# Kernel optimization log

Hardware: AMD Instinct MI355X
Metric: run time of the kernel (lower is better)

Reference implementation:

```python
import jax, jax.numpy as jnp
import numpy as np


def setup_inputs() -> dict:
    key = jax.random.key(0)
    k1, k2, k3 = jax.random.split(key, 3)
    B, N, K, F, H = 4, 50000, 10, 128, 16
    x = jax.random.normal(k1, (B, N, K, F), dtype=jnp.float32)
    # xavier-like scales for learned params
    W = jax.random.normal(k2, (F, 4 * H), dtype=jnp.float32) * (1.0 / np.sqrt(F))
    a = jax.random.normal(k3, (4, H), dtype=jnp.float32) * 0.5
    return {"x": x, "W": W, "a": a}


def reference(x, W, a):
    # x: [B, N, K, F]; W: [F, 4H] (head-major blocks of 4); a: [4, H]
    B, N, K, F = x.shape
    H = a.shape[1]
    Wr = W.reshape(F, H, 4)                              # per-head projection
    hw = jnp.einsum('bnkf,fhd->bnkhd', x, Wr)            # [B,N,K,H,4]
    logits = jnp.einsum('bnkhd,dh->bnkh', hw, a)         # [B,N,K,H]
    attn = jax.nn.softmax(logits, axis=2)                # softmax over K neighbors
    out = jnp.einsum('bnkh,bnkhd->bnhd', attn, hw)       # [B,N,H,4]
    out = jax.nn.leaky_relu(out, negative_slope=0.2)
    out = out.reshape(B, N, H * 4)                       # concat over heads
    return out.transpose(0, 2, 1)                        # [B, 4H, N]
```

## Files before the change

kernel.cpp:

```cpp
#include <hip/hip_runtime.h>

typedef short bf16x8 __attribute__((ext_vector_type(8)));
typedef float f32x4 __attribute__((ext_vector_type(4)));

constexpr int Bc = 4;
constexpr int Nc = 50000;
constexpr int Kc = 10;
constexpr int Fc = 128;
constexpr int Hc = 16;
constexpr int Cc = 64;
constexpr int NODES = Bc * Nc;
constexpr int NPB = 8;
constexpr int ROWS = NPB * Kc;
constexpr int MT = ROWS / 16;
constexpr int BLK = 256;

constexpr int LDS_BYTES = 36864;
constexpr int WT_OFF = 20480;
constexpr int OL_OFF = 21760;

__device__ __forceinline__ unsigned short f2bf(float f) {
    unsigned u = __builtin_bit_cast(unsigned, f);
    return (unsigned short)((u + 0x7fffu + ((u >> 16) & 1u)) >> 16);
}

__global__ __launch_bounds__(256)
void prep_w(const float* __restrict__ W, unsigned short* __restrict__ wt) {
    const int t = threadIdx.x;
#pragma unroll
    for (int i = 0; i < 32; ++i) {
        const int flat = t + i * 256;
        const int c = flat & 63;
        const int f = flat >> 6;
        wt[c * 128 + (f ^ ((c & 7) << 3))] = f2bf(W[flat]);
    }
}

__global__ __launch_bounds__(BLK)
void gat_kernel(const float* __restrict__ x,
                const unsigned short* __restrict__ wt_ws,
                const float* __restrict__ a,
                float* __restrict__ out)
{
    __shared__ __align__(16) char smem[LDS_BYTES];

    const int t = threadIdx.x;

    {
        const float4* xg = reinterpret_cast<const float4*>(x + (size_t)blockIdx.x * (ROWS * Fc));
#pragma unroll
        for (int i = 0; i < (ROWS * Fc / 4) / BLK; ++i) {
            const int idx = t + i * BLK;
            const int row = idx >> 5;
            const int f4  = idx & 31;
            const float4 v = xg[idx];
            const unsigned lo = (unsigned)f2bf(v.x) | ((unsigned)f2bf(v.y) << 16);
            const unsigned hi = (unsigned)f2bf(v.z) | ((unsigned)f2bf(v.w) << 16);
            const int byt = (f4 * 8) ^ ((row & 7) << 4);
            *reinterpret_cast<uint2*>(smem + row * 256 + byt) = make_uint2(lo, hi);
        }
        const float4* wg = reinterpret_cast<const float4*>(wt_ws);
#pragma unroll
        for (int i = 0; i < 4; ++i)
            *reinterpret_cast<float4*>(smem + WT_OFF + t * 16 + i * 4096) = wg[t + i * BLK];
    }
    __syncthreads();

    const int w  = t >> 6;
    const int l  = t & 63;
    const int lr = l & 15;
    const int lk = l >> 4;

    bf16x8 bfrag[4];
    {
        const int c = w * 16 + lr;
        const char* wrow = smem + WT_OFF + c * 256;
        const int sw = (c & 7) << 4;
#pragma unroll
        for (int kc = 0; kc < 4; ++kc)
            bfrag[kc] = *reinterpret_cast<const bf16x8*>(wrow + ((kc * 64 + lk * 16) ^ sw));
    }

    f32x4 acc[MT];
#pragma unroll
    for (int m = 0; m < MT; ++m) acc[m] = (f32x4){0.f, 0.f, 0.f, 0.f};

#pragma unroll
    for (int m = 0; m < MT; ++m) {
        const int row = m * 16 + lr;
        const char* xrow = smem + row * 256;
        const int sw = (row & 7) << 4;
#pragma unroll
        for (int kc = 0; kc < 4; ++kc) {
            const bf16x8 af = *reinterpret_cast<const bf16x8*>(xrow + ((kc * 64 + lk * 16) ^ sw));
            acc[m] = __builtin_amdgcn_mfma_f32_16x16x32_bf16(af, bfrag[kc], acc[m], 0, 0, 0);
        }
    }
    __syncthreads();

    {
        float* hw = reinterpret_cast<float*>(smem);
        const int col = w * 16 + lr;
#pragma unroll
        for (int m = 0; m < MT; ++m) {
            const int rbase = m * 16 + lk * 4;
#pragma unroll
            for (int r = 0; r < 4; ++r)
                hw[(rbase + r) * 68 + col] = acc[m][r];
        }
    }
    __syncthreads();

    const float* hw = reinterpret_cast<const float*>(smem);
    float* ol = reinterpret_cast<float*>(smem + OL_OFF);
    if (t < NPB * Hc) {
        const int h  = t & 15;
        const int ln = t >> 4;
        const float ar0 = a[0 * Hc + h];
        const float ar1 = a[1 * Hc + h];
        const float ar2 = a[2 * Hc + h];
        const float ar3 = a[3 * Hc + h];

        float4 hv[Kc];
        float  lg[Kc];
        float  mx = -1e30f;
#pragma unroll
        for (int k = 0; k < Kc; ++k) {
            hv[k] = *reinterpret_cast<const float4*>(hw + (ln * Kc + k) * 68 + h * 4);
            lg[k] = fmaf(hv[k].x, ar0, fmaf(hv[k].y, ar1, fmaf(hv[k].z, ar2, hv[k].w * ar3)));
            mx = fmaxf(mx, lg[k]);
        }
        float lsum = 0.f, o0 = 0.f, o1 = 0.f, o2 = 0.f, o3 = 0.f;
#pragma unroll
        for (int k = 0; k < Kc; ++k) {
            const float p = __expf(lg[k] - mx);
            lsum += p;
            o0 = fmaf(p, hv[k].x, o0);
            o1 = fmaf(p, hv[k].y, o1);
            o2 = fmaf(p, hv[k].z, o2);
            o3 = fmaf(p, hv[k].w, o3);
        }
        const float inv = 1.f / lsum;
        o0 *= inv; o1 *= inv; o2 *= inv; o3 *= inv;
        o0 = fmaxf(o0, 0.2f * o0);
        o1 = fmaxf(o1, 0.2f * o1);
        o2 = fmaxf(o2, 0.2f * o2);
        o3 = fmaxf(o3, 0.2f * o3);
        *reinterpret_cast<float4*>(ol + ln * 68 + h * 4) = make_float4(o0, o1, o2, o3);
    }
    __syncthreads();

    if (t < 128) {
        const int c  = t >> 1;
        const int nq = t & 1;
        const int nb = blockIdx.x * NPB;
        const int b  = nb / Nc;
        const int n0 = nb - b * Nc;
        float4 v;
        v.x = ol[(nq * 4 + 0) * 68 + c];
        v.y = ol[(nq * 4 + 1) * 68 + c];
        v.z = ol[(nq * 4 + 2) * 68 + c];
        v.w = ol[(nq * 4 + 3) * 68 + c];
        *reinterpret_cast<float4*>(out + ((size_t)b * Cc + c) * Nc + n0 + nq * 4) = v;
    }
}

extern "C" void kernel_launch(void* const* d_in, const int* in_sizes, int n_in,
                              void* d_out, int out_size, void* d_ws, size_t ws_size,
                              hipStream_t stream) {
    const float* x = (const float*)d_in[0];
    const float* W = (const float*)d_in[1];
    const float* a = (const float*)d_in[2];
    float* out = (float*)d_out;
    unsigned short* wt = (unsigned short*)d_ws;

    prep_w<<<1, 256, 0, stream>>>(W, wt);
    gat_kernel<<<NODES / NPB, BLK, 0, stream>>>(x, wt, a, out);
}
```

Measured before the change: 233.6 us.

## Load x directly from global into MFMA fragments, skipping LDS staging

Each wave now reads its x rows straight from global memory into registers, converts them to bf16 and feeds the MFMA. The shared-memory staging pass and one barrier are gone. W is pre-laid out in fragment order so each lane loads its B fragments directly from global, and prep_w is spread across 32 blocks. Launch bounds request 4 blocks per CU. The trade-off is that every wave reads all 16 rows across lanes with 32-byte strided accesses, so global coalescing is weaker, and all four waves redundantly read the same x rows and lean on cache.

Measured after the change: 472.0 us. 2.02x slower.

```diff
diff --git a/kernel.cpp b/kernel.cpp
--- a/kernel.cpp
+++ b/kernel.cpp
@@ -15,57 +15,42 @@
 constexpr int MT = ROWS / 16;
 constexpr int BLK = 256;
 
-constexpr int LDS_BYTES = 36864;
-constexpr int WT_OFF = 20480;
-constexpr int OL_OFF = 21760;
-
 __device__ __forceinline__ unsigned short f2bf(float f) {
     unsigned u = __builtin_bit_cast(unsigned, f);
     return (unsigned short)((u + 0x7fffu + ((u >> 16) & 1u)) >> 16);
 }
 
+__device__ __forceinline__ bf16x8 cvt8(float4 a, float4 b) {
+    bf16x8 r;
+    r[0] = (short)f2bf(a.x); r[1] = (short)f2bf(a.y);
+    r[2] = (short)f2bf(a.z); r[3] = (short)f2bf(a.w);
+    r[4] = (short)f2bf(b.x); r[5] = (short)f2bf(b.y);
+    r[6] = (short)f2bf(b.z); r[7] = (short)f2bf(b.w);
+    return r;
+}
+
 __global__ __launch_bounds__(256)
 void prep_w(const float* __restrict__ W, unsigned short* __restrict__ wt) {
-    const int t = threadIdx.x;
-#pragma unroll
-    for (int i = 0; i < 32; ++i) {
-        const int flat = t + i * 256;
-        const int c = flat & 63;
-        const int f = flat >> 6;
-        wt[c * 128 + (f ^ ((c & 7) << 3))] = f2bf(W[flat]);
-    }
+    const int dst = blockIdx.x * 256 + threadIdx.x;
+    const int j  = dst & 7;
+    const int kc = (dst >> 3) & 3;
+    const int l  = (dst >> 5) & 63;
+    const int w  = dst >> 11;
+    const int c  = w * 16 + (l & 15);
+    const int f  = kc * 32 + (l >> 4) * 8 + j;
+    wt[dst] = f2bf(W[f * 64 + c]);
 }
 
-__global__ __launch_bounds__(BLK)
+__global__ __launch_bounds__(BLK, 4)
 void gat_kernel(const float* __restrict__ x,
                 const unsigned short* __restrict__ wt_ws,
                 const float* __restrict__ a,
                 float* __restrict__ out)
 {
-    __shared__ __align__(16) char smem[LDS_BYTES];
+    __shared__ float hw[ROWS * 68];
+    __shared__ float ol[NPB * 68];
 
-    const int t = threadIdx.x;
-
-    {
-        const float4* xg = reinterpret_cast<const float4*>(x + (size_t)blockIdx.x * (ROWS * Fc));
-#pragma unroll
-        for (int i = 0; i < (ROWS * Fc / 4) / BLK; ++i) {
-            const int idx = t + i * BLK;
-            const int row = idx >> 5;
-            const int f4  = idx & 31;
-            const float4 v = xg[idx];
-            const unsigned lo = (unsigned)f2bf(v.x) | ((unsigned)f2bf(v.y) << 16);
-            const unsigned hi = (unsigned)f2bf(v.z) | ((unsigned)f2bf(v.w) << 16);
-            const int byt = (f4 * 8) ^ ((row & 7) << 4);
-            *reinterpret_cast<uint2*>(smem + row * 256 + byt) = make_uint2(lo, hi);
-        }
-        const float4* wg = reinterpret_cast<const float4*>(wt_ws);
-#pragma unroll
-        for (int i = 0; i < 4; ++i)
-            *reinterpret_cast<float4*>(smem + WT_OFF + t * 16 + i * 4096) = wg[t + i * BLK];
-    }
-    __syncthreads();
-
+    const int t  = threadIdx.x;
     const int w  = t >> 6;
     const int l  = t & 63;
     const int lr = l & 15;
@@ -73,33 +58,31 @@
 
     bf16x8 bfrag[4];
     {
-        const int c = w * 16 + lr;
-        const char* wrow = smem + WT_OFF + c * 256;
-        const int sw = (c & 7) << 4;
+        const bf16x8* wp = reinterpret_cast<const bf16x8*>(wt_ws + w * 2048 + l * 32);
 #pragma unroll
-        for (int kc = 0; kc < 4; ++kc)
-            bfrag[kc] = *reinterpret_cast<const bf16x8*>(wrow + ((kc * 64 + lk * 16) ^ sw));
+        for (int kc = 0; kc < 4; ++kc) bfrag[kc] = wp[kc];
     }
 
     f32x4 acc[MT];
 #pragma unroll
     for (int m = 0; m < MT; ++m) acc[m] = (f32x4){0.f, 0.f, 0.f, 0.f};
 
+    const float* xb = x + ((size_t)blockIdx.x * ROWS + lr) * Fc + lk * 8;
 #pragma unroll
     for (int m = 0; m < MT; ++m) {
-        const int row = m * 16 + lr;
-        const char* xrow = smem + row * 256;
-        const int sw = (row & 7) << 4;
+        const float* ap = xb + (size_t)m * 16 * Fc;
+        float4 u[4], v[4];
 #pragma unroll
         for (int kc = 0; kc < 4; ++kc) {
-            const bf16x8 af = *reinterpret_cast<const bf16x8*>(xrow + ((kc * 64 + lk * 16) ^ sw));
-            acc[m] = __builtin_amdgcn_mfma_f32_16x16x32_bf16(af, bfrag[kc], acc[m], 0, 0, 0);
+            u[kc] = *reinterpret_cast<const float4*>(ap + kc * 32);
+            v[kc] = *reinterpret_cast<const float4*>(ap + kc * 32 + 4);
         }
+#pragma unroll
+        for (int kc = 0; kc < 4; ++kc)
+            acc[m] = __builtin_amdgcn_mfma_f32_16x16x32_bf16(cvt8(u[kc], v[kc]), bfrag[kc], acc[m], 0, 0, 0);
     }
-    __syncthreads();
 
     {
-        float* hw = reinterpret_cast<float*>(smem);
         const int col = w * 16 + lr;
 #pragma unroll
         for (int m = 0; m < MT; ++m) {
@@ -111,8 +94,6 @@
     }
     __syncthreads();
 
-    const float* hw = reinterpret_cast<const float*>(smem);
-    float* ol = reinterpret_cast<float*>(smem + OL_OFF);
     if (t < NPB * Hc) {
         const int h  = t & 15;
         const int ln = t >> 4;
@@ -174,6 +155,6 @@
     float* out = (float*)d_out;
     unsigned short* wt = (unsigned short*)d_ws;
 
-    prep_w<<<1, 256, 0, stream>>>(W, wt);
+    prep_w<<<32, 256, 0, stream>>>(W, wt);
     gat_kernel<<<NODES / NPB, BLK, 0, stream>>>(x, wt, a, out);
 }
```
